# Performance work log

Measured on AMD Instinct MI355X. Metric: run time of the kernel, lower is better.

## Reference

```python
import jax, jax.numpy as jnp
import numpy as np

H = 2048          # hidden_size
I = 2048          # per-expert intermediate = 6144 // (topk=2 + share=1)
E_ROUTED = 7      # num_experts - num_share_experts
NS = 1            # num_share_experts
TOPK = 2
TEMP = 1.0


def setup_inputs() -> dict:
    key = jax.random.key(0)
    ks = jax.random.split(key, 20)
    s = lambda fan_in: 1.0 / np.sqrt(fan_in)
    inp = {
        "x": jax.random.normal(ks[0], (4, 1024, H), dtype=jnp.float32),
        # router (nn.Linear(H, E_ROUTED)) + learnable gate bias (init zeros)
        "Wr": jax.random.normal(ks[1], (H, E_ROUTED), jnp.float32) * s(H),
        "br": jax.random.normal(ks[2], (E_ROUTED,), jnp.float32) * s(H),
        "gate_bias": jnp.zeros((E_ROUTED,), jnp.float32),
        # stacked routed-expert FFN params (up -> SwiGLU gate -> down)
        "Wup": jax.random.normal(ks[3], (E_ROUTED, H, I), jnp.float32) * s(H),
        "bup": jax.random.normal(ks[4], (E_ROUTED, I), jnp.float32) * s(H),
        "Wgate": jax.random.normal(ks[5], (E_ROUTED, I, I), jnp.float32) * s(I),
        "bgate": jax.random.normal(ks[6], (E_ROUTED, I), jnp.float32) * s(I),
        "Wdown": jax.random.normal(ks[7], (E_ROUTED, I, H), jnp.float32) * s(I),
        "bdown": jax.random.normal(ks[8], (E_ROUTED, H), jnp.float32) * s(I),
        # shared expert: share_up Linear(H, NS*I), SwiGLU(I), share_down Linear(I, H)
        "Wsu": jax.random.normal(ks[9], (H, NS * I), jnp.float32) * s(H),
        "bsu": jax.random.normal(ks[10], (NS * I,), jnp.float32) * s(H),
        "Wsg": jax.random.normal(ks[11], (I, I), jnp.float32) * s(I),
        "bsg": jax.random.normal(ks[12], (I,), jnp.float32) * s(I),
        "Wsd": jax.random.normal(ks[13], (I, H), jnp.float32) * s(I),
        "bsd": jax.random.normal(ks[14], (H,), jnp.float32) * s(I),
    }
    return inp


def _moe_forward(x, Wr, br, gate_bias, Wup, bup, Wgate, bgate, Wdown, bdown,
                 Wsu, bsu, Wsg, bsg, Wsd, bsd):
    B, S, _ = x.shape
    xt = x.reshape(-1, H)                                   # [N, H]
    N = xt.shape[0]

    # ---- router: top-k gating with scatter(-inf) + softmax over all routed experts
    gate = (xt @ Wr + br) / TEMP                            # [N, E]
    bias_gate = gate + gate_bias
    _, ids = jax.lax.top_k(bias_gate, TOPK)                 # [N, K]
    sel_logits = jnp.take_along_axis(gate, ids, axis=-1)    # [N, K] (unbiased logits)
    masked = jnp.full_like(gate, -jnp.inf)
    masked = masked.at[jnp.arange(N)[:, None], ids].set(sel_logits)
    probs = jax.nn.softmax(masked, axis=-1)                 # [N, E], zero off top-k

    # ---- routed experts: dense grouped FFN, combine weighted by probs
    # (probs are exactly 0 for unselected experts, matching the masked
    #  gather / scatter-add combine in the original loop)
    u = jnp.einsum('nh,ehi->eni', xt, Wup) + bup[:, None, :]            # [E, N, I]
    g = jax.nn.silu(jnp.einsum('eni,eij->enj', u, Wgate) + bgate[:, None, :]) * u
    eo = jnp.einsum('enj,ejh->enh', g, Wdown) + bdown[:, None, :]       # [E, N, H]
    out = jnp.einsum('ne,enh->nh', probs, eo)                           # [N, H]

    # ---- shared expert(s)
    su = (xt @ Wsu + bsu).reshape(N, NS, I)                 # [N, NS, I]
    sg = jax.nn.silu(su @ Wsg + bsg) * su                   # SwiGLU
    so = (sg @ Wsd + bsd).sum(axis=1)                       # [N, H]
    out = out + so

    return out.reshape(B, S, H)


def reference(x, Wr, br, gate_bias, Wup, bup, Wgate, bgate, Wdown, bdown,
              Wsu, bsu, Wsg, bsg, Wsd, bsd):
    return _moe_forward(x, Wr, br, gate_bias, Wup, bup, Wgate, bgate,
                        Wdown, bdown, Wsu, bsu, Wsg, bsg, Wsd, bsd)
```

## Files before the change

### kernel.cpp

```cpp
#include <hip/hip_runtime.h>
#include <stdint.h>

#define HD 2048
#define NTOK 4096
#define NROUTED 7
#define NEXP 8
#define ROWS_ROUTED 8192
#define ROWS_TOTAL 12288
#define ROWS_PAD 12416

#define BM 256
#define BN 256
#define BK 32
#define NT (HD / BK)

typedef __attribute__((ext_vector_type(8))) __bf16 bf16x8;
typedef __attribute__((ext_vector_type(4))) float f32x4;
typedef __attribute__((ext_vector_type(8))) unsigned short u16x8;

__device__ __forceinline__ float bf2f(unsigned short h) {
  union { unsigned int u; float f; } x; x.u = ((unsigned int)h) << 16; return x.f;
}
__device__ __forceinline__ unsigned short f2bf(float f) {
  union { float f; unsigned int u; } x; x.f = f;
  unsigned int r = x.u + 0x7fffu + ((x.u >> 16) & 1u);
  return (unsigned short)(r >> 16);
}

__device__ __forceinline__ void async16(const void* g, void* l) {
  __builtin_amdgcn_global_load_lds(
      (__attribute__((address_space(1))) const void*)(uintptr_t)g,
      (__attribute__((address_space(3))) void*)(unsigned int)(uintptr_t)l,
      16, 0, 0);
}

__global__ __launch_bounds__(256) void k_convert_bf16(const float* __restrict__ in,
                                                      unsigned short* __restrict__ out, int n) {
  int i = (blockIdx.x * 256 + threadIdx.x) * 4;
  if (i >= n) return;
  float4 v = *(const float4*)(in + i);
  ushort4 o; o.x = f2bf(v.x); o.y = f2bf(v.y); o.z = f2bf(v.z); o.w = f2bf(v.w);
  *(ushort4*)(out + i) = o;
}

__global__ __launch_bounds__(256) void k_transpose_bf16(const float* __restrict__ inR,
                                                        const float* __restrict__ inS,
                                                        unsigned short* __restrict__ outR,
                                                        unsigned short* __restrict__ outS) {
  __shared__ float tile[64][65];
  const size_t bs = (size_t)HD * HD;
  int z = blockIdx.z;
  const float* in = (z < NROUTED) ? (inR + (size_t)z * bs) : inS;
  unsigned short* out = (z < NROUTED) ? (outR + (size_t)z * bs) : outS;
  int tx = threadIdx.x & 15, ty = threadIdx.x >> 4;
  int r0 = blockIdx.y * 64, c0 = blockIdx.x * 64;
  #pragma unroll
  for (int i = 0; i < 4; i++) {
    float4 v = *(const float4*)(in + (size_t)(r0 + ty + 16 * i) * HD + c0 + tx * 4);
    tile[ty + 16 * i][tx * 4 + 0] = v.x;
    tile[ty + 16 * i][tx * 4 + 1] = v.y;
    tile[ty + 16 * i][tx * 4 + 2] = v.z;
    tile[ty + 16 * i][tx * 4 + 3] = v.w;
  }
  __syncthreads();
  #pragma unroll
  for (int i = 0; i < 4; i++) {
    int orow = ty + 16 * i;
    int oc = tx * 4;
    ushort4 o;
    o.x = f2bf(tile[oc + 0][orow]);
    o.y = f2bf(tile[oc + 1][orow]);
    o.z = f2bf(tile[oc + 2][orow]);
    o.w = f2bf(tile[oc + 3][orow]);
    *(ushort4*)(out + (size_t)(c0 + orow) * HD + r0 + oc) = o;
  }
}

__global__ __launch_bounds__(256) void k_router(const float* __restrict__ x, const float* __restrict__ Wr,
                                                const float* __restrict__ br, const float* __restrict__ gbias,
                                                int* __restrict__ ids, float* __restrict__ wts,
                                                int* __restrict__ ctrl) {
  int lane = threadIdx.x & 63, wid = threadIdx.x >> 6;
  int t = blockIdx.x * 4 + wid;
  const float* xr = x + (size_t)t * HD;
  float acc[NROUTED];
  #pragma unroll
  for (int e = 0; e < NROUTED; e++) acc[e] = 0.f;
  for (int k = lane; k < HD; k += 64) {
    float xv = xr[k];
    const float* wrow = Wr + k * NROUTED;
    #pragma unroll
    for (int e = 0; e < NROUTED; e++) acc[e] += xv * wrow[e];
  }
  #pragma unroll
  for (int e = 0; e < NROUTED; e++) {
    #pragma unroll
    for (int off = 32; off > 0; off >>= 1) acc[e] += __shfl_down(acc[e], off);
  }
  if (lane == 0) {
    float lg[NROUTED], bg[NROUTED];
    #pragma unroll
    for (int e = 0; e < NROUTED; e++) { lg[e] = acc[e] + br[e]; bg[e] = lg[e] + gbias[e]; }
    int i1 = 0;
    #pragma unroll
    for (int e = 1; e < NROUTED; e++) if (bg[e] > bg[i1]) i1 = e;
    int i2 = (i1 == 0) ? 1 : 0;
    #pragma unroll
    for (int e = 0; e < NROUTED; e++) if (e != i1 && bg[e] > bg[i2]) i2 = e;
    float l1 = lg[i1], l2 = lg[i2];
    float m = fmaxf(l1, l2);
    float p1 = __expf(l1 - m), p2 = __expf(l2 - m);
    float s = p1 + p2;
    ids[2*t] = i1; ids[2*t+1] = i2;
    wts[2*t] = p1 / s; wts[2*t+1] = p2 / s;
    atomicAdd(&ctrl[i1], 1); atomicAdd(&ctrl[i2], 1);
  }
}

__global__ void k_offsets(int* ctrl) {
  if (threadIdx.x == 0 && blockIdx.x == 0) {
    ctrl[7] = NTOK;
    int o = 0;
    #pragma unroll
    for (int e = 0; e < NEXP; e++) { ctrl[8 + e] = o; o += ctrl[e]; }
  }
}

__global__ __launch_bounds__(256) void k_build_lists(const int* __restrict__ ids, int* __restrict__ ctrl,
                                                     int* __restrict__ tok_list, int* __restrict__ tok_pos) {
  int t = blockIdx.x * 256 + threadIdx.x;
  if (t >= NTOK) return;
  #pragma unroll
  for (int j = 0; j < 2; j++) {
    int e = ids[2*t + j];
    int pos = ctrl[8 + e] + atomicAdd(&ctrl[16 + e], 1);
    tok_list[pos] = t;
    tok_pos[2*t + j] = pos;
  }
  tok_list[ROWS_ROUTED + t] = t;
}


#define STAGE(bufp)                                                       \
  { unsigned short* _a = &sm[bufp][0][0];                                 \
    unsigned short* _b = &sm[bufp][1][0];                                 \
    _Pragma("unroll")                                                     \
    for (int r = 0; r < 2; r++) {                                         \
      async16(pA[r], _a + r * 4096 + wid * 512); pA[r] += BK;             \
      async16(pB[r], _b + r * 4096 + wid * 512); pB[r] += BK;             \
    } }

template<int MODE>
__global__ __launch_bounds__(512, 2) void k_moe_gemm(
    const unsigned short* __restrict__ Abase,
    const unsigned short* __restrict__ WTr,
    const unsigned short* __restrict__ WTs,
    const float* __restrict__ biasR,
    const float* __restrict__ biasS,
    const int* __restrict__ ctrl,
    const int* __restrict__ tok_list,
    const unsigned short* __restrict__ Uep,
    unsigned short* __restrict__ Out)
{
  const int e   = blockIdx.z;
  const int cnt = ctrl[e];
  const int m0  = blockIdx.y * BM;
  if (m0 >= cnt) return;
  const int off = ctrl[8 + e];
  const int n0  = blockIdx.x * BN;

  const unsigned short* W = (e < NROUTED) ? (WTr + (size_t)e * HD * HD) : WTs;
  const float* bias = (e < NROUTED) ? (biasR + e * HD) : biasS;

  __shared__ __align__(16) unsigned short sm[2][2][BM * BK];

  const int tid  = threadIdx.x;
  const int lane = tid & 63;
  const int wid  = tid >> 6;

  const int srow = tid >> 2;
  const int sslot = tid & 3;
  const int csw = (sslot ^ ((srow >> 1) & 3)) * 8;
  const unsigned short* pA[2];
  const unsigned short* pB[2];
  #pragma unroll
  for (int r = 0; r < 2; r++) {
    int row = r * 128 + srow;
    size_t ga;
    if (MODE == 0) {
      int mr = m0 + row; if (mr >= cnt) mr = cnt - 1;
      ga = (size_t)tok_list[off + mr] * HD;
    } else {
      ga = (size_t)(off + m0 + row) * HD;
    }
    pA[r] = Abase + ga + csw;
    pB[r] = W + (size_t)(n0 + row) * HD + csw;
  }

  const int wr   = wid >> 2;
  const int wc   = wid & 3;
  const int rm   = lane & 15;
  const int q    = lane >> 4;
  const int qx   = (q ^ ((rm >> 1) & 3)) * 8;

  f32x4 acc[8][4];
  f32x4 zero = {0.f, 0.f, 0.f, 0.f};
  #pragma unroll
  for (int i = 0; i < 8; i++)
    #pragma unroll
    for (int j = 0; j < 4; j++) acc[i][j] = zero;

  STAGE(0);
  STAGE(1);

  for (int t = 0; t < NT; ++t) {
    const int buf = t & 1;
    if (t < NT - 1) { asm volatile("s_waitcnt vmcnt(4)" ::: "memory"); }
    else           { asm volatile("s_waitcnt vmcnt(0)" ::: "memory"); }
    __builtin_amdgcn_s_barrier();
    __builtin_amdgcn_sched_barrier(0);

    const unsigned short* _ab = &sm[buf][0][0];
    const unsigned short* _bb = &sm[buf][1][0];
    bf16x8 af[8], bfr[4];
    #pragma unroll
    for (int mi = 0; mi < 8; mi++)
      af[mi] = *(const bf16x8*)(_ab + (wr * 128 + mi * 16 + rm) * BK + qx);
    #pragma unroll
    for (int ni = 0; ni < 4; ni++)
      bfr[ni] = *(const bf16x8*)(_bb + (wc * 64 + ni * 16 + rm) * BK + qx);
    #pragma unroll
    for (int mi = 0; mi < 8; mi++)
      #pragma unroll
      for (int ni = 0; ni < 4; ni++)
        acc[mi][ni] = __builtin_amdgcn_mfma_f32_16x16x32_bf16(af[mi], bfr[ni], acc[mi][ni], 0, 0, 0);

    __builtin_amdgcn_sched_barrier(0);
    __builtin_amdgcn_s_barrier();
    __builtin_amdgcn_sched_barrier(0);
    if (t + 2 < NT) STAGE(buf);
  }

  #pragma unroll
  for (int mi = 0; mi < 8; mi++) {
    int rb = wr * 128 + mi * 16 + q * 4;
    #pragma unroll
    for (int r = 0; r < 4; r++) {
      int gm = m0 + rb + r;
      if (gm < cnt) {
        size_t orow = (size_t)(off + gm) * HD;
        #pragma unroll
        for (int ni = 0; ni < 4; ni++) {
          int gn = n0 + wc * 64 + ni * 16 + rm;
          float v = acc[mi][ni][r] + bias[gn];
          if (MODE == 1) {
            float uv = bf2f(Uep[orow + gn]);
            float sg = v / (1.f + __expf(-v));
            v = sg * uv;
          }
          Out[orow + gn] = f2bf(v);
        }
      }
    }
  }
}

__global__ __launch_bounds__(256) void k_combine(const unsigned short* __restrict__ eo,
                                                 const int* __restrict__ tok_pos,
                                                 const float* __restrict__ wts,
                                                 float* __restrict__ out) {
  int t = blockIdx.x;
  int h = threadIdx.x * 8;
  int p0 = tok_pos[2*t], p1 = tok_pos[2*t+1];
  float w0 = wts[2*t], w1 = wts[2*t+1];
  u16x8 a = *(const u16x8*)(eo + (size_t)p0 * HD + h);
  u16x8 b = *(const u16x8*)(eo + (size_t)p1 * HD + h);
  u16x8 c = *(const u16x8*)(eo + (size_t)(ROWS_ROUTED + t) * HD + h);
  float* o = out + (size_t)t * HD + h;
  #pragma unroll
  for (int i = 0; i < 8; i++) o[i] = w0 * bf2f(a[i]) + w1 * bf2f(b[i]) + bf2f(c[i]);
}

extern "C" void kernel_launch(void* const* d_in, const int* in_sizes, int n_in,
                              void* d_out, int out_size, void* d_ws, size_t ws_size,
                              hipStream_t stream) {
  (void)in_sizes; (void)n_in; (void)out_size; (void)ws_size;
  const float* x     = (const float*)d_in[0];
  const float* Wr    = (const float*)d_in[1];
  const float* br    = (const float*)d_in[2];
  const float* gbias = (const float*)d_in[3];
  const float* Wup   = (const float*)d_in[4];
  const float* bup   = (const float*)d_in[5];
  const float* Wgate = (const float*)d_in[6];
  const float* bgate = (const float*)d_in[7];
  const float* Wdown = (const float*)d_in[8];
  const float* bdown = (const float*)d_in[9];
  const float* Wsu   = (const float*)d_in[10];
  const float* bsu   = (const float*)d_in[11];
  const float* Wsg   = (const float*)d_in[12];
  const float* bsg   = (const float*)d_in[13];
  const float* Wsd   = (const float*)d_in[14];
  const float* bsd   = (const float*)d_in[15];
  float* out = (float*)d_out;

  char* ws = (char*)d_ws;
  size_t o = 0;
  auto alloc = [&](size_t bytes) { char* p = ws + o; o += (bytes + 255) & ~(size_t)255; return p; };
  unsigned short* WT_r = (unsigned short*)alloc((size_t)7 * HD * HD * 2);
  unsigned short* WT_s = (unsigned short*)alloc((size_t)HD * HD * 2);
  unsigned short* xbf  = (unsigned short*)alloc((size_t)NTOK * HD * 2);
  unsigned short* bufU = (unsigned short*)alloc((size_t)ROWS_PAD * HD * 2);
  unsigned short* bufG = (unsigned short*)alloc((size_t)ROWS_PAD * HD * 2);
  int*   ctrl     = (int*)alloc(4096);
  int*   ids      = (int*)alloc(NTOK * 2 * 4);
  float* wts      = (float*)alloc(NTOK * 2 * 4);
  int*   tok_list = (int*)alloc(ROWS_TOTAL * 4);
  int*   tok_pos  = (int*)alloc(NTOK * 2 * 4);

  hipMemsetAsync(ctrl, 0, 96, stream);
  k_convert_bf16<<<NTOK * HD / 1024, 256, 0, stream>>>(x, xbf, NTOK * HD);
  k_router<<<NTOK / 4, 256, 0, stream>>>(x, Wr, br, gbias, ids, wts, ctrl);
  k_offsets<<<1, 64, 0, stream>>>(ctrl);
  k_build_lists<<<NTOK / 256, 256, 0, stream>>>(ids, ctrl, tok_list, tok_pos);

  dim3 tgrid(HD / 64, HD / 64, NEXP);
  dim3 ggrid(HD / BN, 4096 / BM, NEXP);

  k_transpose_bf16<<<tgrid, 256, 0, stream>>>(Wup, Wsu, WT_r, WT_s);
  k_moe_gemm<0><<<ggrid, 512, 0, stream>>>(xbf, WT_r, WT_s, bup, bsu, ctrl, tok_list, nullptr, bufU);

  k_transpose_bf16<<<tgrid, 256, 0, stream>>>(Wgate, Wsg, WT_r, WT_s);
  k_moe_gemm<1><<<ggrid, 512, 0, stream>>>(bufU, WT_r, WT_s, bgate, bsg, ctrl, tok_list, bufU, bufG);

  k_transpose_bf16<<<tgrid, 256, 0, stream>>>(Wdown, Wsd, WT_r, WT_s);
  k_moe_gemm<2><<<ggrid, 512, 0, stream>>>(bufG, WT_r, WT_s, bdown, bsd, ctrl, tok_list, nullptr, bufU);

  k_combine<<<NTOK, 256, 0, stream>>>(bufU, tok_pos, wts, out);
}
```

Before: 1.222 ms.

## Double K-tile depth and interleave LDS reads, MFMA and prefetch in quadrants

Raises the GEMM K tile from 32 to 64 and moves LDS to 128 KB of dynamic shared memory with an 8-way XOR swizzle. The main loop is split into four quadrant phases so LDS fragment loads, MFMA bursts at raised wave priority, and the next-stage global-to-LDS prefetches for A and B interleave, in the style of a ping-pong schedule. The goal is fewer barriers per unit of K and better overlap of memory and matrix work. In exchange it adds many more s_barriers per iteration and uses 128 KB of LDS per block, which may cut occupancy from the 2 blocks per CU that launch_bounds asks for.

```diff
diff --git a/kernel.cpp b/kernel.cpp
--- a/kernel.cpp
+++ b/kernel.cpp
@@ -11,7 +11,7 @@
 
 #define BM 256
 #define BN 256
-#define BK 32
+#define BK 64
 #define NT (HD / BK)
 
 typedef __attribute__((ext_vector_type(8))) __bf16 bf16x8;
@@ -141,14 +141,50 @@
 }
 
 
-#define STAGE(bufp)                                                       \
-  { unsigned short* _a = &sm[bufp][0][0];                                 \
-    unsigned short* _b = &sm[bufp][1][0];                                 \
+#define STAGE_A(bufp)                                                     \
+  { unsigned short* _d = smA + (bufp) * 16384 + wid * 512;                \
+    async16(pA[0], _d);        async16(pA[1], _d + 4096);                 \
+    async16(pA[2], _d + 8192); async16(pA[3], _d + 12288);                \
+    pA[0] += BK; pA[1] += BK; pA[2] += BK; pA[3] += BK; }
+
+#define STAGE_B(bufp)                                                     \
+  { unsigned short* _d = smB + (bufp) * 16384 + wid * 512;                \
+    async16(pB[0], _d);        async16(pB[1], _d + 4096);                 \
+    async16(pB[2], _d + 8192); async16(pB[3], _d + 12288);                \
+    pB[0] += BK; pB[1] += BK; pB[2] += BK; pB[3] += BK; }
+
+#define LDA(bufp, a)                                                      \
+  { const unsigned short* _p = smA + (bufp) * 16384;                      \
     _Pragma("unroll")                                                     \
-    for (int r = 0; r < 2; r++) {                                         \
-      async16(pA[r], _a + r * 4096 + wid * 512); pA[r] += BK;             \
-      async16(pB[r], _b + r * 4096 + wid * 512); pB[r] += BK;             \
+    for (int mi2 = 0; mi2 < 4; mi2++) {                                   \
+      _Pragma("unroll")                                                   \
+      for (int ks = 0; ks < 2; ks++)                                      \
+        af[mi2][ks] = *(const bf16x8*)(_p                                 \
+            + (wr * 128 + (a) * 64 + mi2 * 16 + rm) * 64                  \
+            + (((ks * 4 + q) ^ s7) * 8));                                 \
     } }
+
+#define LDB(bufp, nh, dst)                                                \
+  { const unsigned short* _p = smB + (bufp) * 16384;                      \
+    _Pragma("unroll")                                                     \
+    for (int ni2 = 0; ni2 < 2; ni2++) {                                   \
+      _Pragma("unroll")                                                   \
+      for (int ks = 0; ks < 2; ks++)                                      \
+        dst[ni2][ks] = *(const bf16x8*)(_p                                \
+            + (wc * 64 + (nh) * 32 + ni2 * 16 + rm) * 64                  \
+            + (((ks * 4 + q) ^ s7) * 8));                                 \
+    } }
+
+#define MM(a, nh, Bf)                                                     \
+  { _Pragma("unroll")                                                     \
+    for (int mi2 = 0; mi2 < 4; mi2++) {                                   \
+      _Pragma("unroll")                                                   \
+      for (int ni2 = 0; ni2 < 2; ni2++) {                                 \
+        acc[(a)*4+mi2][(nh)*2+ni2] = __builtin_amdgcn_mfma_f32_16x16x32_bf16( \
+            af[mi2][0], Bf[ni2][0], acc[(a)*4+mi2][(nh)*2+ni2], 0, 0, 0); \
+        acc[(a)*4+mi2][(nh)*2+ni2] = __builtin_amdgcn_mfma_f32_16x16x32_bf16( \
+            af[mi2][1], Bf[ni2][1], acc[(a)*4+mi2][(nh)*2+ni2], 0, 0, 0); \
+      } } }
 
 template<int MODE>
 __global__ __launch_bounds__(512, 2) void k_moe_gemm(
@@ -172,20 +208,21 @@
   const unsigned short* W = (e < NROUTED) ? (WTr + (size_t)e * HD * HD) : WTs;
   const float* bias = (e < NROUTED) ? (biasR + e * HD) : biasS;
 
-  __shared__ __align__(16) unsigned short sm[2][2][BM * BK];
+  extern __shared__ unsigned short smem[];
+  unsigned short* smA = smem;
+  unsigned short* smB = smem + 32768;
 
   const int tid  = threadIdx.x;
   const int lane = tid & 63;
   const int wid  = tid >> 6;
 
-  const int srow = tid >> 2;
-  const int sslot = tid & 3;
-  const int csw = (sslot ^ ((srow >> 1) & 3)) * 8;
-  const unsigned short* pA[2];
-  const unsigned short* pB[2];
-  #pragma unroll
-  for (int r = 0; r < 2; r++) {
-    int row = r * 128 + srow;
+  const int srow = tid >> 3;
+  const int csw  = ((tid & 7) ^ (srow & 7)) * 8;
+  const unsigned short* pA[4];
+  const unsigned short* pB[4];
+  #pragma unroll
+  for (int r = 0; r < 4; r++) {
+    int row = r * 64 + srow;
     size_t ga;
     if (MODE == 0) {
       int mr = m0 + row; if (mr >= cnt) mr = cnt - 1;
@@ -197,11 +234,11 @@
     pB[r] = W + (size_t)(n0 + row) * HD + csw;
   }
 
-  const int wr   = wid >> 2;
-  const int wc   = wid & 3;
-  const int rm   = lane & 15;
-  const int q    = lane >> 4;
-  const int qx   = (q ^ ((rm >> 1) & 3)) * 8;
+  const int wr = wid >> 2;
+  const int wc = wid & 3;
+  const int rm = lane & 15;
+  const int q  = lane >> 4;
+  const int s7 = rm & 7;
 
   f32x4 acc[8][4];
   f32x4 zero = {0.f, 0.f, 0.f, 0.f};
@@ -210,35 +247,44 @@
     #pragma unroll
     for (int j = 0; j < 4; j++) acc[i][j] = zero;
 
-  STAGE(0);
-  STAGE(1);
+  bf16x8 af[4][2], bf0[2][2], bf1[2][2];
+
+  STAGE_A(0); STAGE_B(0);
+  STAGE_A(1); STAGE_B(1);
 
   for (int t = 0; t < NT; ++t) {
     const int buf = t & 1;
-    if (t < NT - 1) { asm volatile("s_waitcnt vmcnt(4)" ::: "memory"); }
-    else           { asm volatile("s_waitcnt vmcnt(0)" ::: "memory"); }
-    __builtin_amdgcn_s_barrier();
-    __builtin_amdgcn_sched_barrier(0);
-
-    const unsigned short* _ab = &sm[buf][0][0];
-    const unsigned short* _bb = &sm[buf][1][0];
-    bf16x8 af[8], bfr[4];
-    #pragma unroll
-    for (int mi = 0; mi < 8; mi++)
-      af[mi] = *(const bf16x8*)(_ab + (wr * 128 + mi * 16 + rm) * BK + qx);
-    #pragma unroll
-    for (int ni = 0; ni < 4; ni++)
-      bfr[ni] = *(const bf16x8*)(_bb + (wc * 64 + ni * 16 + rm) * BK + qx);
-    #pragma unroll
-    for (int mi = 0; mi < 8; mi++)
-      #pragma unroll
-      for (int ni = 0; ni < 4; ni++)
-        acc[mi][ni] = __builtin_amdgcn_mfma_f32_16x16x32_bf16(af[mi], bfr[ni], acc[mi][ni], 0, 0, 0);
-
-    __builtin_amdgcn_sched_barrier(0);
-    __builtin_amdgcn_s_barrier();
-    __builtin_amdgcn_sched_barrier(0);
-    if (t + 2 < NT) STAGE(buf);
+    if (t < NT - 1) { asm volatile("s_waitcnt vmcnt(8)" ::: "memory"); }
+    else            { asm volatile("s_waitcnt vmcnt(0)" ::: "memory"); }
+    __builtin_amdgcn_s_barrier();
+    __builtin_amdgcn_sched_barrier(0);
+
+    LDA(buf, 0); LDB(buf, 0, bf0);
+    __builtin_amdgcn_s_barrier();
+    asm volatile("s_waitcnt lgkmcnt(0)" ::: "memory");
+    __builtin_amdgcn_sched_barrier(0);
+    __builtin_amdgcn_s_setprio(1); MM(0, 0, bf0); __builtin_amdgcn_s_setprio(0);
+    __builtin_amdgcn_s_barrier();
+
+    LDB(buf, 1, bf1);
+    __builtin_amdgcn_s_barrier();
+    asm volatile("s_waitcnt lgkmcnt(0)" ::: "memory");
+    __builtin_amdgcn_sched_barrier(0);
+    __builtin_amdgcn_s_setprio(1); MM(0, 1, bf1); __builtin_amdgcn_s_setprio(0);
+    __builtin_amdgcn_s_barrier();
+
+    LDA(buf, 1);
+    if (t + 2 < NT) STAGE_B(buf);
+    __builtin_amdgcn_s_barrier();
+    asm volatile("s_waitcnt lgkmcnt(0)" ::: "memory");
+    __builtin_amdgcn_sched_barrier(0);
+    __builtin_amdgcn_s_setprio(1); MM(1, 1, bf1); __builtin_amdgcn_s_setprio(0);
+    __builtin_amdgcn_s_barrier();
+
+    if (t + 2 < NT) STAGE_A(buf);
+    __builtin_amdgcn_s_barrier();
+    __builtin_amdgcn_sched_barrier(0);
+    __builtin_amdgcn_s_setprio(1); MM(1, 0, bf0); __builtin_amdgcn_s_setprio(0);
   }
 
   #pragma unroll
@@ -317,6 +363,17 @@
   int*   tok_list = (int*)alloc(ROWS_TOTAL * 4);
   int*   tok_pos  = (int*)alloc(NTOK * 2 * 4);
 
+  static bool attr_done = false;
+  if (!attr_done) {
+    hipFuncSetAttribute(reinterpret_cast<const void*>(&k_moe_gemm<0>),
+                        hipFuncAttributeMaxDynamicSharedMemorySize, 131072);
+    hipFuncSetAttribute(reinterpret_cast<const void*>(&k_moe_gemm<1>),
+                        hipFuncAttributeMaxDynamicSharedMemorySize, 131072);
+    hipFuncSetAttribute(reinterpret_cast<const void*>(&k_moe_gemm<2>),
+                        hipFuncAttributeMaxDynamicSharedMemorySize, 131072);
+    attr_done = true;
+  }
+
   hipMemsetAsync(ctrl, 0, 96, stream);
   k_convert_bf16<<<NTOK * HD / 1024, 256, 0, stream>>>(x, xbf, NTOK * HD);
   k_router<<<NTOK / 4, 256, 0, stream>>>(x, Wr, br, gbias, ids, wts, ctrl);
@@ -327,13 +384,13 @@
   dim3 ggrid(HD / BN, 4096 / BM, NEXP);
 
   k_transpose_bf16<<<tgrid, 256, 0, stream>>>(Wup, Wsu, WT_r, WT_s);
-  k_moe_gemm<0><<<ggrid, 512, 0, stream>>>(xbf, WT_r, WT_s, bup, bsu, ctrl, tok_list, nullptr, bufU);
+  k_moe_gemm<0><<<ggrid, 512, 131072, stream>>>(xbf, WT_r, WT_s, bup, bsu, ctrl, tok_list, nullptr, bufU);
 
   k_transpose_bf16<<<tgrid, 256, 0, stream>>>(Wgate, Wsg, WT_r, WT_s);
-  k_moe_gemm<1><<<ggrid, 512, 0, stream>>>(bufU, WT_r, WT_s, bgate, bsg, ctrl, tok_list, bufU, bufG);
+  k_moe_gemm<1><<<ggrid, 512, 131072, stream>>>(bufU, WT_r, WT_s, bgate, bsg, ctrl, tok_list, bufU, bufG);
 
   k_transpose_bf16<<<tgrid, 256, 0, stream>>>(Wdown, Wsd, WT_r, WT_s);
-  k_moe_gemm<2><<<ggrid, 512, 0, stream>>>(bufG, WT_r, WT_s, bdown, bsd, ctrl, tok_list, nullptr, bufU);
+  k_moe_gemm<2><<<ggrid, 512, 131072, stream>>>(bufG, WT_r, WT_s, bdown, bsd, ctrl, tok_list, nullptr, bufU);
 
   k_combine<<<NTOK, 256, 0, stream>>>(bufU, tok_pos, wts, out);
 }
```

Result: faster. 1.139 ms (-6.8%).
